# Kernel tuning notes

Hardware: AMD Instinct MI355X
Metric: run time of the kernel (lower is better)

The kernel has to match this reference:

```python
import jax, jax.numpy as jnp
import numpy as np

MAX_SEQ = 512
HIDDEN = 1024
E = 2 * HIDDEN  # expansion
S = 128         # head dim s
EPS = 1e-5


def setup_inputs() -> dict:
    key = jax.random.key(0)
    ks = jax.random.split(key, 10)
    B, N = 32, 512
    x = jax.random.normal(ks[0], (B, N, HIDDEN), dtype=jnp.float32)
    attention_mask = jnp.ones((B, N), dtype=jnp.float32)
    gamma = jax.random.uniform(ks[1], (2, S), dtype=jnp.float32)
    beta = jax.random.uniform(ks[2], (2, S), dtype=jnp.float32)
    w = jax.random.uniform(ks[3], (2 * MAX_SEQ - 1,), dtype=jnp.float32)
    a_p = jax.random.uniform(ks[4], (1, S), dtype=jnp.float32)
    b_p = jax.random.uniform(ks[5], (1, S), dtype=jnp.float32)
    # uv: Linear(hidden -> 2e+s), stored input-major for x @ uv_w
    uv_w = jax.random.normal(ks[6], (HIDDEN, 2 * E + S), dtype=jnp.float32) * 0.02
    uv_b = jnp.zeros((2 * E + S,), dtype=jnp.float32)
    o_w = jax.random.normal(ks[7], (E, HIDDEN), dtype=jnp.float32) * 0.02
    o_b = jnp.zeros((HIDDEN,), dtype=jnp.float32)
    ln_g = jnp.ones((HIDDEN,), dtype=jnp.float32)
    ln_b = jnp.zeros((HIDDEN,), dtype=jnp.float32)
    return {"x": x, "attention_mask": attention_mask, "gamma": gamma, "beta": beta,
            "w": w, "a_p": a_p, "b_p": b_p, "uv_w": uv_w, "uv_b": uv_b,
            "o_w": o_w, "o_b": o_b, "ln_g": ln_g, "ln_b": ln_b}


def _rope_seq(x):
    # x: [b, n, 2, s]; rotary positions along axis 1 (matches module's rope(x, dim=1))
    n, d = x.shape[1], x.shape[-1]
    half = d // 2
    pos = jnp.arange(n, dtype=jnp.float32)
    # inv_freq = 10000 ** (arange(half)/half)  (freq_seq = -arange/half, inv = 10000**-freq_seq)
    inv_freq = jnp.power(10000.0, jnp.arange(half, dtype=jnp.float32) / half)
    sinusoid = pos[:, None] * inv_freq  # [n, half]
    sin = jnp.sin(sinusoid)[None, :, None, :]
    cos = jnp.cos(sinusoid)[None, :, None, :]
    x1, x2 = jnp.split(x, 2, axis=-1)
    return jnp.concatenate([x1 * cos - x2 * sin, x2 * cos + x1 * sin], axis=-1)


def _rel_pos_bias(w, seq_len):
    # Toeplitz trick (max_seq_length <= 512 path)
    t = jnp.pad(w[: 2 * MAX_SEQ - 1], (0, MAX_SEQ))          # [3S-1]
    t = jnp.tile(t, MAX_SEQ)[: -MAX_SEQ].reshape(-1, MAX_SEQ, 3 * MAX_SEQ - 2)
    r = (2 * MAX_SEQ - 1) // 2
    t = t[..., r:-r]                                          # [1, S, S]
    return t[:, :seq_len, :seq_len]


def reference(x, attention_mask, gamma, beta, w, a_p, b_p, uv_w, uv_b, o_w, o_b, ln_g, ln_b):
    n = x.shape[1]
    shortcut = x
    mu = jnp.mean(x, axis=-1, keepdims=True)
    var = jnp.mean(jnp.square(x - mu), axis=-1, keepdims=True)
    xn = (x - mu) * jax.lax.rsqrt(var + EPS) * ln_g + ln_b
    uv = jax.nn.silu(xn @ uv_w + uv_b)                        # [b, n, 2e+s]
    u, v, base = jnp.split(uv, [E, 2 * E], axis=-1)
    base = base[..., None, :] * gamma + beta                  # [b, n, 2, s]
    base = _rope_seq(base)
    q, k = base[:, :, 0], base[:, :, 1]                       # [b, n, s]
    qk = jnp.einsum('bnd,bmd->bnm', q, k)
    qk = qk + ((1.0 - attention_mask) * -1e12)[:, None, :]
    bias = _rel_pos_bias(w, n)                                # [1, n, n]
    kernel = jnp.square(jax.nn.relu(qk / MAX_SEQ + bias))
    out = u * jnp.einsum('bnm,bme->bne', kernel, v)           # [b, n, e]
    return out @ o_w + o_b + shortcut
```

## Files before the change

kernel.cpp:

```cpp
#include <hip/hip_runtime.h>
#include <math.h>

#define HIDDEN 1024
#define NSEQ   512
#define BATCH  32
#define EDIM   2048
#define SDIM   128
#define UVN    (2 * EDIM + SDIM)

using short8  = __attribute__((ext_vector_type(8))) short;
using float4x = __attribute__((ext_vector_type(4))) float;

__device__ __forceinline__ ushort f2bf(float f) {
    unsigned u = __float_as_uint(f);
    u += 0x7FFFu + ((u >> 16) & 1u);
    return (ushort)(u >> 16);
}
__device__ __forceinline__ float bf2f(ushort h) {
    return __uint_as_float(((unsigned)h) << 16);
}

#define ASYNC16(gp, lp) __builtin_amdgcn_global_load_lds( \
    (const __attribute__((address_space(1))) unsigned int*)(unsigned long long)(const void*)(gp), \
    (__attribute__((address_space(3))) unsigned int*)(unsigned int)(unsigned long long)(const void*)(lp), \
    16, 0, 0)

__global__ __launch_bounds__(64) void tab_kernel(float* __restrict__ sin_t,
                                                 float* __restrict__ cos_t) {
    int i = blockIdx.x;
    int j = threadIdx.x;
    double inv = pow(10000.0, (double)j / 64.0);
    double ang = (double)i * inv;
    sin_t[i * 64 + j] = (float)sin(ang);
    cos_t[i * 64 + j] = (float)cos(ang);
}

__global__ __launch_bounds__(256) void transpose_f32_bf16(const float* __restrict__ src,
                                                          ushort* __restrict__ dst,
                                                          int R, int Cc) {
    __shared__ float tile[32][33];
    const int bx = blockIdx.x;
    const int by = blockIdx.y;
    const int lx = threadIdx.x & 31;
    const int gy = threadIdx.x >> 5;
#pragma unroll
    for (int i = 0; i < 4; ++i) {
        int r = by * 32 + gy + i * 8;
        tile[gy + i * 8][lx] = src[(size_t)r * Cc + bx * 32 + lx];
    }
    __syncthreads();
#pragma unroll
    for (int i = 0; i < 4; ++i) {
        int c = bx * 32 + gy + i * 8;
        dst[(size_t)c * R + by * 32 + lx] = f2bf(tile[lx][gy + i * 8]);
    }
}

__global__ __launch_bounds__(256) void ln_kernel(const float* __restrict__ x,
                                                 const float* __restrict__ g,
                                                 const float* __restrict__ b,
                                                 ushort* __restrict__ xn) {
    const size_t t = blockIdx.x;
    const int tid = threadIdx.x;
    const float4 v = ((const float4*)(x + t * HIDDEN))[tid];
    float s = v.x + v.y + v.z + v.w;
#pragma unroll
    for (int off = 32; off > 0; off >>= 1) s += __shfl_down(s, off);
    __shared__ float red[4];
    const int wid = tid >> 6, lane = tid & 63;
    if (lane == 0) red[wid] = s;
    __syncthreads();
    const float mean = (red[0] + red[1] + red[2] + red[3]) * (1.0f / HIDDEN);
    __syncthreads();
    const float dx = v.x - mean, dy = v.y - mean, dz = v.z - mean, dw = v.w - mean;
    float s2 = dx * dx + dy * dy + dz * dz + dw * dw;
#pragma unroll
    for (int off = 32; off > 0; off >>= 1) s2 += __shfl_down(s2, off);
    if (lane == 0) red[wid] = s2;
    __syncthreads();
    const float var = (red[0] + red[1] + red[2] + red[3]) * (1.0f / HIDDEN);
    const float rs = rsqrtf(var + 1e-5f);
    const float4 gv = ((const float4*)g)[tid];
    const float4 bv = ((const float4*)b)[tid];
    ushort4 o;
    o.x = f2bf(dx * rs * gv.x + bv.x);
    o.y = f2bf(dy * rs * gv.y + bv.y);
    o.z = f2bf(dz * rs * gv.z + bv.z);
    o.w = f2bf(dw * rs * gv.w + bv.w);
    ((ushort4*)(xn + t * HIDDEN))[tid] = o;
}

__device__ __forceinline__ void mfma_core_128(const ushort* __restrict__ A,
                                              const ushort* __restrict__ Bt,
                                              const int lda, const int ldb, const int K,
                                              const int m0, const int n0,
                                              ushort* As, ushort* Bs,
                                              float4x (&acc)[4][4]) {
    const int tid = threadIdx.x;
    const int l = tid & 63, w = tid >> 6;
    const int wm = (w & 1) << 6, wn = (w >> 1) << 6;

    const int c0 = w * 128 + l;
    const int r0 = c0 >> 2, kc0 = (c0 & 3) * 8;
    const int c1 = c0 + 64;
    const int r1 = c1 >> 2, kc1 = (c1 & 3) * 8;
    char* ldsA0 = (char*)As + (size_t)(w * 128) * 16;
    char* ldsA1 = ldsA0 + 1024;
    char* ldsB0 = (char*)Bs + (size_t)(w * 128) * 16;
    char* ldsB1 = ldsB0 + 1024;
    const ushort* gA0 = A + (size_t)(m0 + r0) * lda + kc0;
    const ushort* gA1 = A + (size_t)(m0 + r1) * lda + kc1;
    const ushort* gB0 = Bt + (size_t)(n0 + r0) * ldb + kc0;
    const ushort* gB1 = Bt + (size_t)(n0 + r1) * ldb + kc1;

    const int lr = l & 15, lk = (l >> 4) * 8;
    int aoff[4], boff[4];
#pragma unroll
    for (int i = 0; i < 4; ++i) {
        aoff[i] = (wm + i * 16 + lr) * 32 + lk;
        boff[i] = (wn + i * 16 + lr) * 32 + lk;
    }

    for (int k0 = 0; k0 < K; k0 += 32) {
        __syncthreads();
        ASYNC16(gA0 + k0, ldsA0);
        ASYNC16(gA1 + k0, ldsA1);
        ASYNC16(gB0 + k0, ldsB0);
        ASYNC16(gB1 + k0, ldsB1);
        __syncthreads();
        short8 af[4], bfr[4];
#pragma unroll
        for (int i = 0; i < 4; ++i) af[i] = *(const short8*)(As + aoff[i]);
#pragma unroll
        for (int i = 0; i < 4; ++i) bfr[i] = *(const short8*)(Bs + boff[i]);
#pragma unroll
        for (int mi = 0; mi < 4; ++mi)
#pragma unroll
            for (int ni = 0; ni < 4; ++ni)
                acc[mi][ni] = __builtin_amdgcn_mfma_f32_16x16x32_bf16(
                    af[mi], bfr[ni], acc[mi][ni], 0, 0, 0);
    }
}

template <typename F>
__device__ __forceinline__ void epilogue_loop(const float4x (&acc)[4][4],
                                              int m0, int n0, F body) {
    const int l = threadIdx.x & 63, w = threadIdx.x >> 6;
    const int wm = (w & 1) << 6, wn = (w >> 1) << 6;
    const int lrow = (l >> 4) << 2, lcol = l & 15;
#pragma unroll
    for (int mi = 0; mi < 4; ++mi)
#pragma unroll
        for (int ni = 0; ni < 4; ++ni)
#pragma unroll
            for (int r = 0; r < 4; ++r) {
                const int m = m0 + wm + mi * 16 + lrow + r;
                const int n = n0 + wn + ni * 16 + lcol;
                body(m, n, acc[mi][ni][r]);
            }
}

__global__ __launch_bounds__(256) void gemm_uv_mfma(const ushort* __restrict__ A,
                                                    const ushort* __restrict__ Bt,
                                                    const float* __restrict__ bias,
                                                    ushort* __restrict__ U,
                                                    ushort* __restrict__ VT,
                                                    float* __restrict__ BASE) {
    __shared__ ushort As[128 * 32], Bs[128 * 32];
    float4x acc[4][4] = {};
    const int n0 = blockIdx.x * 128, m0 = blockIdx.y * 128;
    mfma_core_128(A, Bt, HIDDEN, HIDDEN, HIDDEN, m0, n0, As, Bs, acc);
    const int bx = blockIdx.x;
    if (bx < 16) {
        epilogue_loop(acc, m0, n0, [&](int m, int n, float aval) {
            float val = aval + bias[n];
            val = val / (1.0f + expf(-val));
            U[(size_t)m * EDIM + n] = f2bf(val);
        });
    } else if (bx < 32) {
        epilogue_loop(acc, m0, n0, [&](int m, int n, float aval) {
            float val = aval + bias[n];
            val = val / (1.0f + expf(-val));
            const int e = n - EDIM;
            const int b = m >> 9;
            const int s = m & (NSEQ - 1);
            VT[((size_t)b * EDIM + e) * NSEQ + s] = f2bf(val);
        });
    } else {
        epilogue_loop(acc, m0, n0, [&](int m, int n, float aval) {
            float val = aval + bias[n];
            val = val / (1.0f + expf(-val));
            BASE[(size_t)m * SDIM + (n - 2 * EDIM)] = val;
        });
    }
}

__global__ __launch_bounds__(128) void rope_kernel(const float* __restrict__ base,
                                                   const float* __restrict__ gamma,
                                                   const float* __restrict__ beta,
                                                   const float* __restrict__ sin_t,
                                                   const float* __restrict__ cos_t,
                                                   float* __restrict__ q,
                                                   float* __restrict__ k) {
    const size_t t = blockIdx.x;
    const int d = threadIdx.x;
    const int pos = (int)(t & (NSEQ - 1));
    __shared__ float vq[128], vk[128];
    const float bval = base[t * SDIM + d];
    vq[d] = bval * gamma[d] + beta[d];
    vk[d] = bval * gamma[SDIM + d] + beta[SDIM + d];
    __syncthreads();
    const int h = d & 63;
    const float sn = sin_t[pos * 64 + h];
    const float cs = cos_t[pos * 64 + h];
    float oq, ok;
    if (d < 64) {
        oq = vq[d] * cs - vq[d + 64] * sn;
        ok = vk[d] * cs - vk[d + 64] * sn;
    } else {
        oq = vq[d] * cs + vq[d - 64] * sn;
        ok = vk[d] * cs + vk[d - 64] * sn;
    }
    q[t * SDIM + d] = oq;
    k[t * SDIM + d] = ok;
}

__global__ __launch_bounds__(256) void gemm_qk(const float* __restrict__ q,
                                               const float* __restrict__ k,
                                               const float* __restrict__ mask,
                                               const float* __restrict__ w,
                                               ushort* __restrict__ km) {
    __shared__ float As[16][68];
    __shared__ float Bs[16][68];
    const int b = blockIdx.z;
    const float* A = q + (size_t)b * NSEQ * SDIM;
    const float* B = k + (size_t)b * NSEQ * SDIM;
    const int tid = threadIdx.x;
    const int tx = tid & 15, ty = tid >> 4;
    const int arow = tid >> 2, acol = (tid & 3) << 2;
    const int n0 = blockIdx.x * 64, m0 = blockIdx.y * 64;
    float acc[4][4] = {};
    for (int k0 = 0; k0 < SDIM; k0 += 16) {
        float4 av = *(const float4*)(A + (size_t)(m0 + arow) * SDIM + (k0 + acol));
        float4 bv = *(const float4*)(B + (size_t)(n0 + arow) * SDIM + (k0 + acol));
        As[acol + 0][arow] = av.x; As[acol + 1][arow] = av.y;
        As[acol + 2][arow] = av.z; As[acol + 3][arow] = av.w;
        Bs[acol + 0][arow] = bv.x; Bs[acol + 1][arow] = bv.y;
        Bs[acol + 2][arow] = bv.z; Bs[acol + 3][arow] = bv.w;
        __syncthreads();
#pragma unroll
        for (int kk = 0; kk < 16; ++kk) {
            const float4 a4 = *(const float4*)&As[kk][ty << 2];
            const float4 b4 = *(const float4*)&Bs[kk][tx << 2];
            const float a[4] = {a4.x, a4.y, a4.z, a4.w};
            const float bb[4] = {b4.x, b4.y, b4.z, b4.w};
#pragma unroll
            for (int i = 0; i < 4; ++i)
#pragma unroll
                for (int j = 0; j < 4; ++j)
                    acc[i][j] = fmaf(a[i], bb[j], acc[i][j]);
        }
        __syncthreads();
    }
    const float inv512 = 1.0f / 512.0f;
#pragma unroll
    for (int i = 0; i < 4; ++i) {
        const int ii = m0 + (ty << 2) + i;
#pragma unroll
        for (int j = 0; j < 4; ++j) {
            const int jj = n0 + (tx << 2) + j;
            const float mterm = (1.0f - mask[b * NSEQ + jj]) * -1e12f;
            float val = (acc[i][j] + mterm) * inv512 + w[511 + jj - ii];
            val = fmaxf(val, 0.0f);
            km[(size_t)b * NSEQ * NSEQ + (size_t)ii * NSEQ + jj] = f2bf(val * val);
        }
    }
}

__global__ __launch_bounds__(256) void gemm_pv_mfma(const ushort* __restrict__ km,
                                                    const ushort* __restrict__ vT,
                                                    ushort* __restrict__ ug) {
    __shared__ ushort As[128 * 32], Bs[128 * 32];
    float4x acc[4][4] = {};
    const int b = blockIdx.z;
    const int n0 = blockIdx.x * 128, m0 = blockIdx.y * 128;
    mfma_core_128(km + (size_t)b * NSEQ * NSEQ, vT + (size_t)b * EDIM * NSEQ,
                  NSEQ, NSEQ, NSEQ, m0, n0, As, Bs, acc);
    const size_t tokbase = (size_t)b * NSEQ;
    epilogue_loop(acc, m0, n0, [&](int m, int n, float aval) {
        const size_t idx = (tokbase + m) * EDIM + n;
        ug[idx] = f2bf(bf2f(ug[idx]) * aval);
    });
}

__global__ __launch_bounds__(256) void gemm_out_mfma(const ushort* __restrict__ A,
                                                     const ushort* __restrict__ Bt,
                                                     const float* __restrict__ ob,
                                                     const float* __restrict__ x,
                                                     float* __restrict__ out) {
    __shared__ ushort As[128 * 32], Bs[128 * 32];
    float4x acc[4][4] = {};
    const int n0 = blockIdx.x * 128, m0 = blockIdx.y * 128;
    mfma_core_128(A, Bt, EDIM, EDIM, EDIM, m0, n0, As, Bs, acc);
    epilogue_loop(acc, m0, n0, [&](int m, int n, float aval) {
        out[(size_t)m * HIDDEN + n] = aval + ob[n] + x[(size_t)m * HIDDEN + n];
    });
}

extern "C" void kernel_launch(void* const* d_in, const int* in_sizes, int n_in,
                              void* d_out, int out_size, void* d_ws, size_t ws_size,
                              hipStream_t stream) {
    const float* x     = (const float*)d_in[0];
    const float* mask  = (const float*)d_in[1];
    const float* gamma = (const float*)d_in[2];
    const float* beta  = (const float*)d_in[3];
    const float* w     = (const float*)d_in[4];
    const float* uv_w  = (const float*)d_in[7];
    const float* uv_b  = (const float*)d_in[8];
    const float* o_w   = (const float*)d_in[9];
    const float* o_b   = (const float*)d_in[10];
    const float* ln_g  = (const float*)d_in[11];
    const float* ln_b  = (const float*)d_in[12];
    float* out = (float*)d_out;

    int C = 32;
    while (C > 1) {
        unsigned long long need = (unsigned long long)C * 5505024ull + 13107200ull;
        if (need <= (unsigned long long)ws_size) break;
        C >>= 1;
    }
    const int R = C * NSEQ;

    char* p = (char*)d_ws;
    ushort* xn  = (ushort*)p;  p += (size_t)C * 1048576;
    ushort* u   = (ushort*)p;  p += (size_t)C * 2097152;
    ushort* vT  = (ushort*)p;  p += (size_t)C * 2097152;
    float* base = (float*)p;   p += (size_t)C * 262144;
    float* sint = (float*)p;   p += 131072;
    float* cost = (float*)p;   p += 131072;
    ushort* uv_wt = (ushort*)p; p += 8650752;
    ushort* o_wt  = (ushort*)p; p += 4194304;
    float* q  = (float*)xn;
    float* k  = (float*)((char*)xn + (size_t)C * 262144);
    ushort* km = (ushort*)((char*)xn + (size_t)C * 524288);

    hipLaunchKernelGGL(tab_kernel, dim3(512), dim3(64), 0, stream, sint, cost);
    hipLaunchKernelGGL(transpose_f32_bf16, dim3(132, 32), dim3(256), 0, stream,
                       uv_w, uv_wt, HIDDEN, UVN);
    hipLaunchKernelGGL(transpose_f32_bf16, dim3(32, 64), dim3(256), 0, stream,
                       o_w, o_wt, EDIM, HIDDEN);

    for (int b0 = 0; b0 < BATCH; b0 += C) {
        const float* xc = x + (size_t)b0 * NSEQ * HIDDEN;
        float*       oc = out + (size_t)b0 * NSEQ * HIDDEN;
        const float* mc = mask + (size_t)b0 * NSEQ;
        hipLaunchKernelGGL(ln_kernel, dim3(R), dim3(256), 0, stream, xc, ln_g, ln_b, xn);
        hipLaunchKernelGGL(gemm_uv_mfma, dim3(33, R / 128), dim3(256), 0, stream,
                           xn, uv_wt, uv_b, u, vT, base);
        hipLaunchKernelGGL(rope_kernel, dim3(R), dim3(128), 0, stream,
                           base, gamma, beta, sint, cost, q, k);
        hipLaunchKernelGGL(gemm_qk, dim3(8, 8, C), dim3(256), 0, stream, q, k, mc, w, km);
        hipLaunchKernelGGL(gemm_pv_mfma, dim3(16, 4, C), dim3(256), 0, stream, km, vT, u);
        hipLaunchKernelGGL(gemm_out_mfma, dim3(8, R / 128), dim3(256), 0, stream,
                           u, o_wt, o_b, xc, oc);
    }
}
```

Before: 604.8 us.

## Double-buffer LDS tiles in MFMA GEMM core and coalesce V-transpose stores

The shared GEMM main loop now prefetches the next K-slice into a second LDS buffer with async global-to-LDS loads while MFMAs run on the current buffer. This drops one barrier per iteration and overlaps global latency with compute. The V-transpose epilogue of the uv GEMM now stages the tile through padded LDS and writes VT with 16-byte coalesced stores instead of strided scalar stores. LDS use per block doubles, which may lower occupancy.

```diff
diff --git a/kernel.cpp b/kernel.cpp
--- a/kernel.cpp
+++ b/kernel.cpp
@@ -121,24 +121,33 @@
         boff[i] = (wn + i * 16 + lr) * 32 + lk;
     }
 
+    ASYNC16(gA0, ldsA0);
+    ASYNC16(gA1, ldsA1);
+    ASYNC16(gB0, ldsB0);
+    ASYNC16(gB1, ldsB1);
+
+    int bufel = 0;
     for (int k0 = 0; k0 < K; k0 += 32) {
         __syncthreads();
-        ASYNC16(gA0 + k0, ldsA0);
-        ASYNC16(gA1 + k0, ldsA1);
-        ASYNC16(gB0 + k0, ldsB0);
-        ASYNC16(gB1 + k0, ldsB1);
-        __syncthreads();
+        const int nb = 8192 - bufel * 2;
+        if (k0 + 32 < K) {
+            ASYNC16(gA0 + k0 + 32, ldsA0 + nb);
+            ASYNC16(gA1 + k0 + 32, ldsA1 + nb);
+            ASYNC16(gB0 + k0 + 32, ldsB0 + nb);
+            ASYNC16(gB1 + k0 + 32, ldsB1 + nb);
+        }
         short8 af[4], bfr[4];
 #pragma unroll
-        for (int i = 0; i < 4; ++i) af[i] = *(const short8*)(As + aoff[i]);
-#pragma unroll
-        for (int i = 0; i < 4; ++i) bfr[i] = *(const short8*)(Bs + boff[i]);
+        for (int i = 0; i < 4; ++i) af[i] = *(const short8*)(As + bufel + aoff[i]);
+#pragma unroll
+        for (int i = 0; i < 4; ++i) bfr[i] = *(const short8*)(Bs + bufel + boff[i]);
 #pragma unroll
         for (int mi = 0; mi < 4; ++mi)
 #pragma unroll
             for (int ni = 0; ni < 4; ++ni)
                 acc[mi][ni] = __builtin_amdgcn_mfma_f32_16x16x32_bf16(
                     af[mi], bfr[ni], acc[mi][ni], 0, 0, 0);
+        bufel ^= 4096;
     }
 }
 
@@ -160,13 +169,16 @@
             }
 }
 
+#define TSTRIDE 132
 __global__ __launch_bounds__(256) void gemm_uv_mfma(const ushort* __restrict__ A,
                                                     const ushort* __restrict__ Bt,
                                                     const float* __restrict__ bias,
                                                     ushort* __restrict__ U,
                                                     ushort* __restrict__ VT,
                                                     float* __restrict__ BASE) {
-    __shared__ ushort As[128 * 32], Bs[128 * 32];
+    __shared__ ushort smem[16384];
+    ushort* As = smem;
+    ushort* Bs = smem + 8192;
     float4x acc[4][4] = {};
     const int n0 = blockIdx.x * 128, m0 = blockIdx.y * 128;
     mfma_core_128(A, Bt, HIDDEN, HIDDEN, HIDDEN, m0, n0, As, Bs, acc);
@@ -178,14 +190,40 @@
             U[(size_t)m * EDIM + n] = f2bf(val);
         });
     } else if (bx < 32) {
-        epilogue_loop(acc, m0, n0, [&](int m, int n, float aval) {
-            float val = aval + bias[n];
-            val = val / (1.0f + expf(-val));
-            const int e = n - EDIM;
-            const int b = m >> 9;
-            const int s = m & (NSEQ - 1);
-            VT[((size_t)b * EDIM + e) * NSEQ + s] = f2bf(val);
-        });
+        const int l = threadIdx.x & 63, w = threadIdx.x >> 6;
+        const int wm = (w & 1) << 6;
+        const int lrow = (l >> 4) << 2, lcol = l & 15;
+        const int bb = m0 >> 9;
+        const int s0 = m0 & (NSEQ - 1);
+        const int e0 = n0 - EDIM;
+        __syncthreads();
+#pragma unroll
+        for (int h = 0; h < 2; ++h) {
+            if ((w >> 1) == h) {
+#pragma unroll
+                for (int mi = 0; mi < 4; ++mi)
+#pragma unroll
+                    for (int ni = 0; ni < 4; ++ni)
+#pragma unroll
+                        for (int r = 0; r < 4; ++r) {
+                            const int nl = ni * 16 + lcol;
+                            const int ml = wm + mi * 16 + lrow + r;
+                            float val = acc[mi][ni][r] + bias[n0 + h * 64 + nl];
+                            val = val / (1.0f + expf(-val));
+                            smem[nl * TSTRIDE + ml] = f2bf(val);
+                        }
+            }
+            __syncthreads();
+#pragma unroll
+            for (int it = 0; it < 4; ++it) {
+                const int nl = it * 16 + (threadIdx.x >> 4);
+                const int cc = (threadIdx.x & 15) * 8;
+                const size_t e = (size_t)(e0 + h * 64 + nl);
+                *(short8*)(VT + ((size_t)bb * EDIM + e) * NSEQ + s0 + cc) =
+                    *(const short8*)(smem + nl * TSTRIDE + cc);
+            }
+            __syncthreads();
+        }
     } else {
         epilogue_loop(acc, m0, n0, [&](int m, int n, float aval) {
             float val = aval + bias[n];
@@ -280,7 +318,9 @@
 __global__ __launch_bounds__(256) void gemm_pv_mfma(const ushort* __restrict__ km,
                                                     const ushort* __restrict__ vT,
                                                     ushort* __restrict__ ug) {
-    __shared__ ushort As[128 * 32], Bs[128 * 32];
+    __shared__ ushort smem[16384];
+    ushort* As = smem;
+    ushort* Bs = smem + 8192;
     float4x acc[4][4] = {};
     const int b = blockIdx.z;
     const int n0 = blockIdx.x * 128, m0 = blockIdx.y * 128;
@@ -298,7 +338,9 @@
                                                      const float* __restrict__ ob,
                                                      const float* __restrict__ x,
                                                      float* __restrict__ out) {
-    __shared__ ushort As[128 * 32], Bs[128 * 32];
+    __shared__ ushort smem[16384];
+    ushort* As = smem;
+    ushort* Bs = smem + 8192;
     float4x acc[4][4] = {};
     const int n0 = blockIdx.x * 128, m0 = blockIdx.y * 128;
     mfma_core_128(A, Bt, EDIM, EDIM, EDIM, m0, n0, As, Bs, acc);
```

Result: slower. 647.8 us (+7.1%).
